# Optimization experiments

Hardware: AMD Instinct MI355X
Metric: run time of the kernel (lower is better)

## Reference

```python
import jax, jax.numpy as jnp
import numpy as np

NUM_JOINTS = 24
IN_DIM = 256      # PoseMLP hidden_dim (per-joint input feature)
HID = 128         # MLP default hidden_dim
OUT_DIM = 6
B = 16384

def setup_inputs() -> dict:
    key = jax.random.key(0)
    ks = jax.random.split(key, 7)
    s1 = 1.0 / np.sqrt(IN_DIM)   # torch Linear init scale (uniform bound)
    s2 = 1.0 / np.sqrt(HID)
    return {
        "pose_feat": jax.random.normal(ks[0], (B, NUM_JOINTS, IN_DIM), dtype=jnp.float32),
        # stacked per-joint weights: Linear stores W as (out, in); we keep (in, out)
        "W1": jax.random.uniform(ks[1], (NUM_JOINTS, IN_DIM, HID), minval=-s1, maxval=s1, dtype=jnp.float32),
        "b1": jax.random.uniform(ks[2], (NUM_JOINTS, HID), minval=-s1, maxval=s1, dtype=jnp.float32),
        "W2": jax.random.uniform(ks[3], (NUM_JOINTS, HID, HID), minval=-s2, maxval=s2, dtype=jnp.float32),
        "b2": jax.random.uniform(ks[4], (NUM_JOINTS, HID), minval=-s2, maxval=s2, dtype=jnp.float32),
        "W3": jax.random.uniform(ks[5], (NUM_JOINTS, HID, OUT_DIM), minval=-s2, maxval=s2, dtype=jnp.float32),
        "b3": jax.random.uniform(ks[6], (NUM_JOINTS, OUT_DIM), minval=-s2, maxval=s2, dtype=jnp.float32),
    }

def reference(pose_feat, W1, b1, W2, b2, W3, b3):
    # Batched per-joint MLPs (fuses the 24 independent small MLPs into 3 grouped GEMMs)
    h = jax.nn.relu(jnp.einsum('bji,jih->bjh', pose_feat, W1) + b1)  # [B,24,128]
    h = jax.nn.relu(jnp.einsum('bjh,jhk->bjk', h, W2) + b2)          # [B,24,128]
    out = jnp.einsum('bjh,jho->bjo', h, W3) + b3                     # [B,24,6]
    return out
```

## Files before the change

### kernel.cpp

```cpp
#include <hip/hip_runtime.h>
#include <hip/hip_fp16.h>

typedef _Float16 half_t;
typedef __attribute__((ext_vector_type(8))) _Float16 half8;
typedef __attribute__((ext_vector_type(4))) _Float16 half4;
typedef __attribute__((ext_vector_type(4))) float floatx4;

#define NJ 24
#define IN_DIM 256
#define HID 128
#define OUT_DIM 6
#define BATCH 16384
#define BM 128

#define W1_JSTRIDE (8 * 128 * 32)
#define W2_JSTRIDE (4 * 128 * 32)
#define W3_JSTRIDE (16 * 128)
#define WT1_ELEMS (NJ * W1_JSTRIDE)
#define WT2_ELEMS (NJ * W2_JSTRIDE)
#define WT3_ELEMS (NJ * W3_JSTRIDE)
#define WT2_OFF WT1_ELEMS
#define WT3_OFF (WT1_ELEMS + WT2_ELEMS)
#define B3P_BYTE_OFF ((size_t)(WT1_ELEMS + WT2_ELEMS + WT3_ELEMS) * 2)
#define PREP_TOTAL (WT1_ELEMS + WT2_ELEMS + WT3_ELEMS + NJ * 16)

__global__ void posemlp_prep(const float* __restrict__ W1, const float* __restrict__ W2,
                             const float* __restrict__ W3, const float* __restrict__ b3,
                             half_t* __restrict__ wt, float* __restrict__ b3p) {
    int t = blockIdx.x * 256 + threadIdx.x;
    if (t < WT1_ELEMS) {
        int j = t / W1_JSTRIDE, r = t % W1_JSTRIDE;
        int ks = r / 4096, r2 = r % 4096;
        int n = r2 / 32, kk = r2 % 32, k = ks * 32 + kk;
        wt[t] = (half_t)W1[((size_t)j * IN_DIM + k) * HID + n];
    } else if (t < WT2_OFF + WT2_ELEMS) {
        int u = t - WT2_OFF;
        int j = u / W2_JSTRIDE, r = u % W2_JSTRIDE;
        int ks = r / 4096, r2 = r % 4096;
        int n = r2 / 32, kk = r2 % 32, k = ks * 32 + kk;
        wt[t] = (half_t)W2[((size_t)j * HID + k) * HID + n];
    } else if (t < WT3_OFF + WT3_ELEMS) {
        int u = t - WT3_OFF;
        int j = u / W3_JSTRIDE, r = u % W3_JSTRIDE;
        int n = r / 128, k = r % 128;
        wt[t] = (n < OUT_DIM) ? (half_t)W3[((size_t)j * HID + k) * OUT_DIM + n] : (half_t)0.0f;
    } else if (t < PREP_TOTAL) {
        int u = t - WT3_OFF - WT3_ELEMS;
        int j = u / 16, n = u % 16;
        b3p[u] = (n < OUT_DIM) ? b3[j * OUT_DIM + n] : 0.0f;
    }
}

__device__ inline void gll16(const void* g, void* l) {
    __builtin_amdgcn_global_load_lds(
        (const __attribute__((address_space(1))) unsigned int*)g,
        (__attribute__((address_space(3))) unsigned int*)l, 16, 0, 0);
}

#define VMWAIT(N) asm volatile("s_waitcnt vmcnt(" #N ")" ::: "memory")
#define LGKM0()                                            \
    do {                                                   \
        asm volatile("s_waitcnt lgkmcnt(0)" ::: "memory"); \
        __builtin_amdgcn_sched_barrier(0);                 \
    } while (0)
#define FENCE()                                 \
    do {                                        \
        asm volatile("" ::: "memory");          \
        __builtin_amdgcn_sched_barrier(0);      \
    } while (0)
__device__ inline void barrier_pinned() {
    __builtin_amdgcn_sched_barrier(0);
    __builtin_amdgcn_s_barrier();
    __builtin_amdgcn_sched_barrier(0);
}

__device__ inline half8 lds_read8(const half_t* lds, int r, int k) {
    int byte = r * 256 + k * 2;
    byte ^= (r & 7) << 4;
    return *(const half8*)((const char*)lds + byte);
}
__device__ inline void lds_write4(half_t* lds, int r, int n, half4 v) {
    int byte = r * 256 + n * 2;
    byte ^= (r & 7) << 4;
    *(half4*)((char*)lds + byte) = v;
}

__device__ inline half8 cvt8(floatx4 a, floatx4 b) {
    half8 h;
    h[0] = (_Float16)a[0]; h[1] = (_Float16)a[1]; h[2] = (_Float16)a[2]; h[3] = (_Float16)a[3];
    h[4] = (_Float16)b[0]; h[5] = (_Float16)b[1]; h[6] = (_Float16)b[2]; h[7] = (_Float16)b[3];
    return h;
}

__global__ __launch_bounds__(256, 2) void posemlp_main(
    const float* __restrict__ X, const half_t* __restrict__ wt,
    const float* __restrict__ b1, const float* __restrict__ b2,
    const float* __restrict__ b3p, float* __restrict__ out) {
    __shared__ half_t wbuf[2][8192];
    __shared__ half_t w3buf[2048];
    __shared__ half_t h_lds[BM * HID];

    const int bid0 = blockIdx.x;
    const int bid = (bid0 & 7) * 384 + (bid0 >> 3);
    const int j = bid >> 7;
    const int row0 = (bid & 127) * BM;
    const int tid = threadIdx.x;
    const int w = tid >> 6;
    const int l = tid & 63;
    const int lrow = l & 15;
    const int q = l >> 4;

    const int rb = w * 32 + lrow;
    const float* xr0 = X + ((size_t)(row0 + rb) * NJ + j) * IN_DIM + q * 8;
    const float* xr1 = X + ((size_t)(row0 + rb + 16) * NJ + j) * IN_DIM + q * 8;

    const half_t* w1j = wt + (size_t)j * W1_JSTRIDE;
    const half_t* w2j = wt + WT2_OFF + (size_t)j * W2_JSTRIDE;
    const half_t* w3j = wt + WT3_OFF + (size_t)j * W3_JSTRIDE;

    const int sn = tid >> 2, ss = tid & 3;
    const int wsrc = sn * 32 + (ss ^ ((sn >> 1) & 3)) * 8;

#define STAGE16K(srcbase, dst) do {                                  \
        gll16((srcbase) + wsrc,        (dst) + w * 512);             \
        gll16((srcbase) + 2048 + wsrc, (dst) + 2048 + w * 512);      \
        gll16((srcbase) + 4096 + wsrc, (dst) + 4096 + w * 512);      \
        gll16((srcbase) + 6144 + wsrc, (dst) + 6144 + w * 512); } while (0)

#define L1_STEP(ks, wb) do {                                                \
        half8 bx0 = cvt8(px[(ks) % 3][0][0], px[(ks) % 3][0][1]);           \
        half8 bx1 = cvt8(px[(ks) % 3][1][0], px[(ks) % 3][1][1]);           \
        if ((ks) < 5) {                                                     \
            px[(ks) % 3][0][0] = *(const floatx4*)(xr0 + ((ks) + 3) * 32);  \
            px[(ks) % 3][0][1] = *(const floatx4*)(xr0 + ((ks) + 3) * 32 + 4); \
            px[(ks) % 3][1][0] = *(const floatx4*)(xr1 + ((ks) + 3) * 32);  \
            px[(ks) % 3][1][1] = *(const floatx4*)(xr1 + ((ks) + 3) * 32 + 4); \
        }                                                                   \
        _Pragma("unroll")                                                   \
        for (int nf = 0; nf < 8; ++nf) {                                    \
            const int n = nf * 16 + lrow;                                   \
            half8 a = *(const half8*)&(wb)[n * 32 + (q ^ ((n >> 1) & 3)) * 8]; \
            acc[nf][0] = __builtin_amdgcn_mfma_f32_16x16x32_f16(a, bx0, acc[nf][0], 0, 0, 0); \
            acc[nf][1] = __builtin_amdgcn_mfma_f32_16x16x32_f16(a, bx1, acc[nf][1], 0, 0, 0); \
        }                                                                   \
    } while (0)

#define L2_STEP(ks, wb) do {                                                \
        half8 bh0 = lds_read8(h_lds, w * 32 + lrow,      (ks) * 32 + q * 8); \
        half8 bh1 = lds_read8(h_lds, w * 32 + 16 + lrow, (ks) * 32 + q * 8); \
        _Pragma("unroll")                                                   \
        for (int nf = 0; nf < 8; ++nf) {                                    \
            const int n = nf * 16 + lrow;                                   \
            half8 a = *(const half8*)&(wb)[n * 32 + (q ^ ((n >> 1) & 3)) * 8]; \
            acc2[nf][0] = __builtin_amdgcn_mfma_f32_16x16x32_f16(a, bh0, acc2[nf][0], 0, 0, 0); \
            acc2[nf][1] = __builtin_amdgcn_mfma_f32_16x16x32_f16(a, bh1, acc2[nf][1], 0, 0, 0); \
        }                                                                   \
    } while (0)

    STAGE16K(w1j, wbuf[0]);
    {
        const int tn = tid >> 4, tsl = tid & 15;
        gll16(w3j + tn * 128 + (tsl ^ tn) * 8, &w3buf[w * 512]);
    }
    FENCE();
    STAGE16K(w1j + 8192, wbuf[1]);
    FENCE();
    floatx4 px[3][2][2];
#pragma unroll
    for (int c = 0; c < 3; ++c) {
        px[c][0][0] = *(const floatx4*)(xr0 + c * 32);
        px[c][0][1] = *(const floatx4*)(xr0 + c * 32 + 4);
        px[c][1][0] = *(const floatx4*)(xr1 + c * 32);
        px[c][1][1] = *(const floatx4*)(xr1 + c * 32 + 4);
    }
    FENCE();
    VMWAIT(12);
    barrier_pinned();

    floatx4 acc[8][2] = {};
    L1_STEP(0, (&wbuf[0][0]));
    L1_STEP(1, (&wbuf[0][4096]));
    LGKM0();
    barrier_pinned();
    STAGE16K(w1j + 16384, wbuf[0]);
    FENCE();
    L1_STEP(2, (&wbuf[1][0]));
    L1_STEP(3, (&wbuf[1][4096]));
    LGKM0();
    barrier_pinned();
    STAGE16K(w1j + 24576, wbuf[1]);
    FENCE();
    VMWAIT(12);
    barrier_pinned();
    L1_STEP(4, (&wbuf[0][0]));
    L1_STEP(5, (&wbuf[0][4096]));
    LGKM0();
    barrier_pinned();
    STAGE16K(w2j, wbuf[0]);
    FENCE();
    VMWAIT(8);
    barrier_pinned();
    L1_STEP(6, (&wbuf[1][0]));
    L1_STEP(7, (&wbuf[1][4096]));
    {
        const float* b1j = b1 + j * HID;
#pragma unroll
        for (int nf = 0; nf < 8; ++nf) {
            floatx4 bb = *(const floatx4*)(b1j + nf * 16 + q * 4);
#pragma unroll
            for (int mf = 0; mf < 2; ++mf) {
                floatx4 v = acc[nf][mf];
                half4 hv;
#pragma unroll
                for (int i = 0; i < 4; ++i) hv[i] = (_Float16)fmaxf(v[i] + bb[i], 0.0f);
                lds_write4(h_lds, w * 32 + mf * 16 + lrow, nf * 16 + q * 4, hv);
            }
        }
    }
    LGKM0();
    barrier_pinned();
    STAGE16K(w2j + 8192, wbuf[1]);
    FENCE();
    VMWAIT(4);
    barrier_pinned();

    floatx4 acc2[8][2] = {};
    L2_STEP(0, (&wbuf[0][0]));
    L2_STEP(1, (&wbuf[0][4096]));
    VMWAIT(0);
    barrier_pinned();
    L2_STEP(2, (&wbuf[1][0]));
    L2_STEP(3, (&wbuf[1][4096]));
    {
        const float* b2j = b2 + j * HID;
#pragma unroll
        for (int nf = 0; nf < 8; ++nf) {
            floatx4 bb = *(const floatx4*)(b2j + nf * 16 + q * 4);
#pragma unroll
            for (int mf = 0; mf < 2; ++mf) {
                floatx4 v = acc2[nf][mf];
                half4 hv;
#pragma unroll
                for (int i = 0; i < 4; ++i) hv[i] = (_Float16)fmaxf(v[i] + bb[i], 0.0f);
                lds_write4(h_lds, w * 32 + mf * 16 + lrow, nf * 16 + q * 4, hv);
            }
        }
    }
    FENCE();

    floatx4 acc3[2] = {};
#pragma unroll
    for (int ks = 0; ks < 4; ++ks) {
        half8 a3 = *(const half8*)&w3buf[lrow * 128 + ((ks * 4 + q) ^ lrow) * 8];
        half8 bh0 = lds_read8(h_lds, w * 32 + lrow, ks * 32 + q * 8);
        half8 bh1 = lds_read8(h_lds, w * 32 + 16 + lrow, ks * 32 + q * 8);
        acc3[0] = __builtin_amdgcn_mfma_f32_16x16x32_f16(a3, bh0, acc3[0], 0, 0, 0);
        acc3[1] = __builtin_amdgcn_mfma_f32_16x16x32_f16(a3, bh1, acc3[1], 0, 0, 0);
    }
    {
        floatx4 bb = *(const floatx4*)(b3p + j * 16 + q * 4);
#pragma unroll
        for (int mf = 0; mf < 2; ++mf) {
            const int orow = row0 + w * 32 + mf * 16 + lrow;
            float* op = out + ((size_t)orow * NJ + j) * OUT_DIM;
            floatx4 v = acc3[mf];
            if (q == 0) {
                float2 s0 = {v[0] + bb[0], v[1] + bb[1]};
                float2 s1 = {v[2] + bb[2], v[3] + bb[3]};
                *(float2*)(op + 0) = s0;
                *(float2*)(op + 2) = s1;
            } else if (q == 1) {
                float2 s = {v[0] + bb[0], v[1] + bb[1]};
                *(float2*)(op + 4) = s;
            }
        }
    }
}

extern "C" void kernel_launch(void* const* d_in, const int* in_sizes, int n_in,
                              void* d_out, int out_size, void* d_ws, size_t ws_size,
                              hipStream_t stream) {
    const float* X  = (const float*)d_in[0];
    const float* W1 = (const float*)d_in[1];
    const float* b1 = (const float*)d_in[2];
    const float* W2 = (const float*)d_in[3];
    const float* b2 = (const float*)d_in[4];
    const float* W3 = (const float*)d_in[5];
    const float* b3 = (const float*)d_in[6];
    float* out = (float*)d_out;

    half_t* wt = (half_t*)d_ws;
    float* b3p = (float*)((char*)d_ws + B3P_BYTE_OFF);

    int prep_blocks = (PREP_TOTAL + 255) / 256;
    posemlp_prep<<<prep_blocks, 256, 0, stream>>>(W1, W2, W3, b3, wt, b3p);

    int grid = NJ * (BATCH / BM);
    posemlp_main<<<grid, 256, 0, stream>>>(X, wt, b1, b2, b3p, out);
}
```

Before: 116.6 us.

## Halve weight staging buffers and raise occupancy to three blocks per CU

Shrinks the double-buffered LDS weight staging from 16K to 8K halves per buffer and restructures the layer pipeline into finer per-k-step stages, each with its own barrier and async load. The X prefetch depth drops from three to two stages to cut register use. Launch bounds are raised to three blocks per CU so the smaller LDS and register footprint can let more blocks hide latency. The cost is more barriers and less prefetch depth per block.

```diff
diff --git a/kernel.cpp b/kernel.cpp
--- a/kernel.cpp
+++ b/kernel.cpp
@@ -92,11 +92,11 @@
     return h;
 }
 
-__global__ __launch_bounds__(256, 2) void posemlp_main(
+__global__ __launch_bounds__(256, 3) void posemlp_main(
     const float* __restrict__ X, const half_t* __restrict__ wt,
     const float* __restrict__ b1, const float* __restrict__ b2,
     const float* __restrict__ b3p, float* __restrict__ out) {
-    __shared__ half_t wbuf[2][8192];
+    __shared__ half_t wbuf[2][4096];
     __shared__ half_t w3buf[2048];
     __shared__ half_t h_lds[BM * HID];
 
@@ -121,20 +121,18 @@
     const int sn = tid >> 2, ss = tid & 3;
     const int wsrc = sn * 32 + (ss ^ ((sn >> 1) & 3)) * 8;
 
-#define STAGE16K(srcbase, dst) do {                                  \
+#define STAGE8K(srcbase, dst) do {                                   \
         gll16((srcbase) + wsrc,        (dst) + w * 512);             \
-        gll16((srcbase) + 2048 + wsrc, (dst) + 2048 + w * 512);      \
-        gll16((srcbase) + 4096 + wsrc, (dst) + 4096 + w * 512);      \
-        gll16((srcbase) + 6144 + wsrc, (dst) + 6144 + w * 512); } while (0)
+        gll16((srcbase) + 2048 + wsrc, (dst) + 2048 + w * 512); } while (0)
 
 #define L1_STEP(ks, wb) do {                                                \
-        half8 bx0 = cvt8(px[(ks) % 3][0][0], px[(ks) % 3][0][1]);           \
-        half8 bx1 = cvt8(px[(ks) % 3][1][0], px[(ks) % 3][1][1]);           \
-        if ((ks) < 5) {                                                     \
-            px[(ks) % 3][0][0] = *(const floatx4*)(xr0 + ((ks) + 3) * 32);  \
-            px[(ks) % 3][0][1] = *(const floatx4*)(xr0 + ((ks) + 3) * 32 + 4); \
-            px[(ks) % 3][1][0] = *(const floatx4*)(xr1 + ((ks) + 3) * 32);  \
-            px[(ks) % 3][1][1] = *(const floatx4*)(xr1 + ((ks) + 3) * 32 + 4); \
+        half8 bx0 = cvt8(px[(ks) & 1][0][0], px[(ks) & 1][0][1]);           \
+        half8 bx1 = cvt8(px[(ks) & 1][1][0], px[(ks) & 1][1][1]);           \
+        if ((ks) <= 5) {                                                    \
+            px[(ks) & 1][0][0] = *(const floatx4*)(xr0 + ((ks) + 2) * 32);  \
+            px[(ks) & 1][0][1] = *(const floatx4*)(xr0 + ((ks) + 2) * 32 + 4); \
+            px[(ks) & 1][1][0] = *(const floatx4*)(xr1 + ((ks) + 2) * 32);  \
+            px[(ks) & 1][1][1] = *(const floatx4*)(xr1 + ((ks) + 2) * 32 + 4); \
         }                                                                   \
         _Pragma("unroll")                                                   \
         for (int nf = 0; nf < 8; ++nf) {                                    \
@@ -157,51 +155,45 @@
         }                                                                   \
     } while (0)
 
-    STAGE16K(w1j, wbuf[0]);
+#define STEP_TAIL(NWAIT, srcbase, dst)  \
+        LGKM0();                        \
+        VMWAIT(NWAIT);                  \
+        barrier_pinned();               \
+        STAGE8K((srcbase), (dst));      \
+        FENCE()
+
+    half_t* wA = &wbuf[0][0];
+    half_t* wB = &wbuf[1][0];
+
+    STAGE8K(w1j, wA);
     {
         const int tn = tid >> 4, tsl = tid & 15;
         gll16(w3j + tn * 128 + (tsl ^ tn) * 8, &w3buf[w * 512]);
     }
     FENCE();
-    STAGE16K(w1j + 8192, wbuf[1]);
-    FENCE();
-    floatx4 px[3][2][2];
-#pragma unroll
-    for (int c = 0; c < 3; ++c) {
+    STAGE8K(w1j + 4096, wB);
+    FENCE();
+    floatx4 px[2][2][2];
+#pragma unroll
+    for (int c = 0; c < 2; ++c) {
         px[c][0][0] = *(const floatx4*)(xr0 + c * 32);
         px[c][0][1] = *(const floatx4*)(xr0 + c * 32 + 4);
         px[c][1][0] = *(const floatx4*)(xr1 + c * 32);
         px[c][1][1] = *(const floatx4*)(xr1 + c * 32 + 4);
     }
     FENCE();
-    VMWAIT(12);
+    VMWAIT(11);
     barrier_pinned();
 
     floatx4 acc[8][2] = {};
-    L1_STEP(0, (&wbuf[0][0]));
-    L1_STEP(1, (&wbuf[0][4096]));
-    LGKM0();
-    barrier_pinned();
-    STAGE16K(w1j + 16384, wbuf[0]);
-    FENCE();
-    L1_STEP(2, (&wbuf[1][0]));
-    L1_STEP(3, (&wbuf[1][4096]));
-    LGKM0();
-    barrier_pinned();
-    STAGE16K(w1j + 24576, wbuf[1]);
-    FENCE();
-    VMWAIT(12);
-    barrier_pinned();
-    L1_STEP(4, (&wbuf[0][0]));
-    L1_STEP(5, (&wbuf[0][4096]));
-    LGKM0();
-    barrier_pinned();
-    STAGE16K(w2j, wbuf[0]);
-    FENCE();
-    VMWAIT(8);
-    barrier_pinned();
-    L1_STEP(6, (&wbuf[1][0]));
-    L1_STEP(7, (&wbuf[1][4096]));
+    L1_STEP(0, wA); STEP_TAIL(12, w1j + 2 * 4096, wA);
+    L1_STEP(1, wB); STEP_TAIL(4,  w1j + 3 * 4096, wB);
+    L1_STEP(2, wA); STEP_TAIL(4,  w1j + 4 * 4096, wA);
+    L1_STEP(3, wB); STEP_TAIL(4,  w1j + 5 * 4096, wB);
+    L1_STEP(4, wA); STEP_TAIL(4,  w1j + 6 * 4096, wA);
+    L1_STEP(5, wB); STEP_TAIL(4,  w1j + 7 * 4096, wB);
+    L1_STEP(6, wA); STEP_TAIL(0,  w2j,            wA);
+    L1_STEP(7, wB);
     {
         const float* b1j = b1 + j * HID;
 #pragma unroll
@@ -217,20 +209,14 @@
             }
         }
     }
-    LGKM0();
-    barrier_pinned();
-    STAGE16K(w2j + 8192, wbuf[1]);
-    FENCE();
-    VMWAIT(4);
-    barrier_pinned();
+    STEP_TAIL(0, w2j + 4096, wB);
 
     floatx4 acc2[8][2] = {};
-    L2_STEP(0, (&wbuf[0][0]));
-    L2_STEP(1, (&wbuf[0][4096]));
-    VMWAIT(0);
-    barrier_pinned();
-    L2_STEP(2, (&wbuf[1][0]));
-    L2_STEP(3, (&wbuf[1][4096]));
+    L2_STEP(0, wA); STEP_TAIL(0, w2j + 2 * 4096, wA);
+    L2_STEP(1, wB); STEP_TAIL(0, w2j + 3 * 4096, wB);
+    L2_STEP(2, wA);
+    LGKM0(); VMWAIT(0); barrier_pinned();
+    L2_STEP(3, wB);
     {
         const float* b2j = b2 + j * HID;
 #pragma unroll
```

After: 119.8 us. 1.03x slower.
